# Kernel optimization log

Measured on AMD Instinct MI355X. Metric: run time of the kernel, lower is better.

## Reference

```python
import jax, jax.numpy as jnp
import numpy as np

N, NA, LAYERS = 8, 4, 4
NTOT = N + NA
DIM = 2 ** NTOT
B = 1024

# Diagonal of the fixed CZ brick layer (CZ is diagonal, so one elementwise pass per layer).
# Qubit 0 is the most-significant bit of the state index (tensorcircuit convention).
def _cz_diag():
    idx = np.arange(DIM)
    bits = (idx[None, :] >> (NTOT - 1 - np.arange(NTOT)[:, None])) & 1  # [NTOT, DIM]
    par = np.zeros(DIM, dtype=np.int64)
    for i in range(NTOT // 2):
        par += bits[2 * i] * bits[2 * i + 1]
    for i in range((NTOT - 1) // 2):
        par += bits[2 * i + 1] * bits[2 * i + 2]
    return jnp.asarray(1.0 - 2.0 * (par % 2), dtype=jnp.complex64)

CZ_DIAG = _cz_diag()

def _apply_1q(state, U, q):
    # state: [B, DIM]; apply 2x2 unitary U on qubit q (batched over samples)
    l, r = 2 ** q, 2 ** (NTOT - q - 1)
    s = state.reshape(-1, l, 2, r)
    return jnp.einsum('ij,bljr->blir', U, s).reshape(-1, DIM)

def _back_circuit(state, params):
    # hardware-efficient ansatz: per layer RX,RY on every qubit, then CZ bricks
    for lay in range(LAYERS):
        off = 2 * NTOT * lay
        for q in range(NTOT):
            th = params[off + q] * 0.5
            c = jnp.cos(th).astype(jnp.complex64)
            ms = (-1j) * jnp.sin(th).astype(jnp.complex64)
            Rx = jnp.stack([jnp.stack([c, ms]), jnp.stack([ms, c])])
            state = _apply_1q(state, Rx, q)
            th = params[off + NTOT + q] * 0.5
            c, s = jnp.cos(th), jnp.sin(th)
            Ry = jnp.stack([jnp.stack([c, -s]), jnp.stack([s, c])]).astype(jnp.complex64)
            state = _apply_1q(state, Ry, q)
        state = state * CZ_DIAG
    return state

def setup_inputs() -> dict:
    key = jax.random.key(0)
    k1, k2, k3, k4 = jax.random.split(key, 4)
    return {
        'inputs_re': jax.random.normal(k1, (B, DIM), jnp.float32),
        'inputs_im': jax.random.normal(k2, (B, DIM), jnp.float32),
        'params': jax.random.normal(k3, (2 * NTOT * LAYERS,), jnp.float32),
        'u': jax.random.uniform(k4, (B,), jnp.float32),
    }

def reference(inputs_re, inputs_im, params, u):
    state = (inputs_re + 1j * inputs_im).astype(jnp.complex64)
    full = _back_circuit(state, params)                      # [B, 2^n_tot]
    s3 = full.reshape(B, 2 ** NA, 2 ** N)                    # [B, 2^na, 2^n]
    probs = jnp.sum(s3.real ** 2 + s3.imag ** 2, axis=2)     # ancilla outcome probs
    cdf = jnp.cumsum(probs, axis=1)
    thresh = u * cdf[:, -1]                                  # inverse-CDF multinomial
    m = jnp.argmax(cdf >= thresh[:, None], axis=1)           # [B] sampled outcome
    post = s3[jnp.arange(B), m]                              # [B, 2^n] collapsed state
    norm = jnp.sqrt(jnp.sum(post.real ** 2 + post.imag ** 2, axis=1, keepdims=True))
    post = post / norm
    return jnp.stack([post.real, post.imag], axis=-1)        # [B, 2^n, 2]
```

## Files before the change

### kernel.cpp

```cpp
#include <hip/hip_runtime.h>
#include <math.h>

#define NTOT   12
#define DIM    4096
#define LAYERS 4
#define NB     1024
#define SPAD   4160

typedef float v2f __attribute__((ext_vector_type(2)));

template<int G>
__device__ __forceinline__ void gate_pk64(v2f (&x)[64], v2f P1, v2f P2) {
#pragma unroll
    for (int p = 0; p < 32; ++p) {
        const int j0 = ((p >> G) << (G + 1)) | (p & ((1 << G) - 1));
        const int j1 = j0 | (1 << G);
        const v2f x0 = x[j0], x1 = x[j1];
        v2f t, u;
        asm("v_pk_mul_f32 %0, %1, %2 op_sel:[1,1] op_sel_hi:[1,0] neg_hi:[1,0]"
            : "=v"(t) : "v"(P2), "v"(x1));
        asm("v_pk_fma_f32 %0, %1, %2, %0 op_sel:[1,0,0] op_sel_hi:[1,1,1] neg_lo:[1,0,0] neg_hi:[1,0,0]"
            : "+v"(t) : "v"(P1), "v"(x1));
        asm("v_pk_fma_f32 %0, %1, %2, %0 op_sel:[0,1,0] op_sel_hi:[0,0,1] neg_lo:[1,0,0]"
            : "+v"(t) : "v"(P2), "v"(x0));
        asm("v_pk_fma_f32 %0, %1, %2, %0 op_sel:[0,0,0] op_sel_hi:[0,1,1]"
            : "+v"(t) : "v"(P1), "v"(x0));
        asm("v_pk_mul_f32 %0, %1, %2 op_sel:[0,1] op_sel_hi:[0,0] neg_hi:[1,0]"
            : "=v"(u) : "v"(P2), "v"(x1));
        asm("v_pk_fma_f32 %0, %1, %2, %0 op_sel:[0,0,0] op_sel_hi:[0,1,1]"
            : "+v"(u) : "v"(P1), "v"(x1));
        asm("v_pk_fma_f32 %0, %1, %2, %0 op_sel:[1,1,0] op_sel_hi:[1,0,1] neg_hi:[1,0,0]"
            : "+v"(u) : "v"(P2), "v"(x0));
        asm("v_pk_fma_f32 %0, %1, %2, %0 op_sel:[1,0,0] op_sel_hi:[1,1,1]"
            : "+v"(u) : "v"(P1), "v"(x0));
        x[j0] = t; x[j1] = u;
    }
}

__device__ __forceinline__ void apply6(v2f (&x)[64], const float4* gco, int top) {
    float4 c;
    c = gco[top - 0]; gate_pk64<0>(x, (v2f){c.x, c.y}, (v2f){c.z, c.w});
    c = gco[top - 1]; gate_pk64<1>(x, (v2f){c.x, c.y}, (v2f){c.z, c.w});
    c = gco[top - 2]; gate_pk64<2>(x, (v2f){c.x, c.y}, (v2f){c.z, c.w});
    c = gco[top - 3]; gate_pk64<3>(x, (v2f){c.x, c.y}, (v2f){c.z, c.w});
    c = gco[top - 4]; gate_pk64<4>(x, (v2f){c.x, c.y}, (v2f){c.z, c.w});
    c = gco[top - 5]; gate_pk64<5>(x, (v2f){c.x, c.y}, (v2f){c.z, c.w});
}

__device__ __forceinline__ void applyCZ64(v2f (&x)[64], unsigned long long mask) {
#pragma unroll
    for (int j = 0; j < 64; ++j) {
        const unsigned int w = (j < 32) ? (unsigned int)mask : (unsigned int)(mask >> 32);
        const unsigned int sw = (w << (31 - (j & 31))) & 0x80000000u;
        x[j].x = __uint_as_float(__float_as_uint(x[j].x) ^ sw);
        x[j].y = __uint_as_float(__float_as_uint(x[j].y) ^ sw);
    }
}

#define KPAR 0xB8B7B8484748B848ULL

__global__ __launch_bounds__(64, 1) void qddpm_kernel(
    const float* __restrict__ in_re,
    const float* __restrict__ in_im,
    const float* __restrict__ params,
    const float* __restrict__ uu,
    float* __restrict__ out)
{
    __shared__ v2f    S[SPAD];
    __shared__ float4 gco[48];
    __shared__ float  sprob[16];

    const int b = blockIdx.x;
    const int l = threadIdx.x;
    const float uval = uu[b];

    if (l < 48) {
        const int lay = l / 12, q = l - lay * 12;
        float c1, s1, c2, s2;
        sincosf(params[lay * 24 + q] * 0.5f, &s1, &c1);
        sincosf(params[lay * 24 + 12 + q] * 0.5f, &s2, &c2);
        gco[l] = make_float4(c1 * c2, c1 * s2, s1 * s2, s1 * c2);
    }

    const unsigned long long parl = ((KPAR >> l) & 1ULL) ? ~0ULL : 0ULL;
    const unsigned long long maskQ =
        KPAR ^ parl ^ ((l & 1)  ? 0xFFFFFFFF00000000ULL : 0ULL);
    const unsigned long long maskP =
        KPAR ^ parl ^ ((l & 32) ? 0xAAAAAAAAAAAAAAAAULL : 0ULL);

    v2f x[64];
    v2f acc2 = (v2f){0.0f, 0.0f};

#pragma unroll 1
    for (int lay = 0; lay < LAYERS; ++lay) {
        if (lay == 0) {
            const float* re = in_re + (size_t)b * DIM + l;
            const float* im = in_im + (size_t)b * DIM + l;
#pragma unroll
            for (int j = 0; j < 64; ++j)
                x[j] = (v2f){re[64 * j], im[64 * j]};
        } else {
#pragma unroll
            for (int j = 0; j < 64; ++j) x[j] = S[65 * j + l];
        }
        apply6(x, gco, lay * 12 + 5);
#pragma unroll
        for (int j = 0; j < 64; ++j) S[65 * j + l] = x[j];

#pragma unroll
        for (int j = 0; j < 64; ++j) x[j] = S[65 * l + j];
        apply6(x, gco, lay * 12 + 11);
        applyCZ64(x, maskQ);
        if (lay == LAYERS - 1) {
#pragma unroll
            for (int j = 0; j < 64; ++j) acc2 += x[j] * x[j];
        }
#pragma unroll
        for (int j = 0; j < 64; ++j) S[65 * l + j] = x[j];
    }
    (void)maskP;

    {
        float partial = acc2.x + acc2.y;
        partial += __shfl_down(partial, 2, 4);
        partial += __shfl_down(partial, 1, 4);
        if ((l & 3) == 0) sprob[l >> 2] = partial;
    }

    {
        float cdf[16];
        float a = 0.0f;
#pragma unroll
        for (int i = 0; i < 16; ++i) { a += sprob[i]; cdf[i] = a; }
        const float thresh = uval * a;
        int m = 0;
#pragma unroll
        for (int i = 15; i >= 0; --i) { if (cdf[i] >= thresh) m = i; }
        const float rn = 1.0f / sqrtf(sprob[m]);

        float2* o2 = (float2*)out + (size_t)b * 256;
#pragma unroll
        for (int c = 0; c < 4; ++c) {
            const v2f amp = S[260 * m + 65 * c + l];
            o2[c * 64 + l] = make_float2(amp.x * rn, amp.y * rn);
        }
    }
}

extern "C" void kernel_launch(void* const* d_in, const int* in_sizes, int n_in,
                              void* d_out, int out_size, void* d_ws, size_t ws_size,
                              hipStream_t stream) {
    const float* in_re  = (const float*)d_in[0];
    const float* in_im  = (const float*)d_in[1];
    const float* params = (const float*)d_in[2];
    const float* u      = (const float*)d_in[3];
    float* out = (float*)d_out;
    qddpm_kernel<<<NB, 64, 0, stream>>>(in_re, in_im, params, u, out);
}
```

Measured before the change: 116.9 us.

## Alternate state layout between half-layers to halve LDS transposes

The state is now loaded contiguously per thread with float4 global loads, so each thread starts holding a row instead of a strided column. The layer loop is split into eight half-layer steps that alternate between the two layouts. It transposes through shared memory only once per layer, and the CZ sign mask is picked to match the current layout (maskQ or maskP). This cuts LDS write/read round trips and strided global loads, at the cost of a slightly more complex control flow with runtime layout selection.

```diff
diff --git a/kernel.cpp b/kernel.cpp
--- a/kernel.cpp
+++ b/kernel.cpp
@@ -1,13 +1,12 @@
 #include <hip/hip_runtime.h>
 #include <math.h>
 
-#define NTOT   12
 #define DIM    4096
-#define LAYERS 4
 #define NB     1024
 #define SPAD   4160
 
 typedef float v2f __attribute__((ext_vector_type(2)));
+typedef unsigned long long ull;
 
 template<int G>
 __device__ __forceinline__ void gate_pk64(v2f (&x)[64], v2f P1, v2f P2) {
@@ -37,21 +36,11 @@
     }
 }
 
-__device__ __forceinline__ void apply6(v2f (&x)[64], const float4* gco, int top) {
-    float4 c;
-    c = gco[top - 0]; gate_pk64<0>(x, (v2f){c.x, c.y}, (v2f){c.z, c.w});
-    c = gco[top - 1]; gate_pk64<1>(x, (v2f){c.x, c.y}, (v2f){c.z, c.w});
-    c = gco[top - 2]; gate_pk64<2>(x, (v2f){c.x, c.y}, (v2f){c.z, c.w});
-    c = gco[top - 3]; gate_pk64<3>(x, (v2f){c.x, c.y}, (v2f){c.z, c.w});
-    c = gco[top - 4]; gate_pk64<4>(x, (v2f){c.x, c.y}, (v2f){c.z, c.w});
-    c = gco[top - 5]; gate_pk64<5>(x, (v2f){c.x, c.y}, (v2f){c.z, c.w});
-}
-
-__device__ __forceinline__ void applyCZ64(v2f (&x)[64], unsigned long long mask) {
+__device__ __forceinline__ void applyCZ64(v2f (&x)[64], ull mask) {
 #pragma unroll
     for (int j = 0; j < 64; ++j) {
-        const unsigned int w = (j < 32) ? (unsigned int)mask : (unsigned int)(mask >> 32);
-        const unsigned int sw = (w << (31 - (j & 31))) & 0x80000000u;
+        const unsigned w = (j < 32) ? (unsigned)mask : (unsigned)(mask >> 32);
+        const unsigned sw = (w << (31 - (j & 31))) & 0x80000000u;
         x[j].x = __uint_as_float(__float_as_uint(x[j].x) ^ sw);
         x[j].y = __uint_as_float(__float_as_uint(x[j].y) ^ sw);
     }
@@ -74,6 +63,20 @@
     const int l = threadIdx.x;
     const float uval = uu[b];
 
+    v2f x[64];
+    {
+        const float4* re4 = (const float4*)(in_re + (size_t)b * DIM + l * 64);
+        const float4* im4 = (const float4*)(in_im + (size_t)b * DIM + l * 64);
+#pragma unroll
+        for (int q = 0; q < 16; ++q) {
+            const float4 vr = re4[q];
+            const float4 vi = im4[q];
+            x[4 * q + 0] = (v2f){vr.x, vi.x};
+            x[4 * q + 1] = (v2f){vr.y, vi.y};
+            x[4 * q + 2] = (v2f){vr.z, vi.z};
+            x[4 * q + 3] = (v2f){vr.w, vi.w};
+        }
+    }
     if (l < 48) {
         const int lay = l / 12, q = l - lay * 12;
         float c1, s1, c2, s2;
@@ -81,52 +84,49 @@
         sincosf(params[lay * 24 + 12 + q] * 0.5f, &s2, &c2);
         gco[l] = make_float4(c1 * c2, c1 * s2, s1 * s2, s1 * c2);
     }
-
-    const unsigned long long parl = ((KPAR >> l) & 1ULL) ? ~0ULL : 0ULL;
-    const unsigned long long maskQ =
-        KPAR ^ parl ^ ((l & 1)  ? 0xFFFFFFFF00000000ULL : 0ULL);
-    const unsigned long long maskP =
-        KPAR ^ parl ^ ((l & 32) ? 0xAAAAAAAAAAAAAAAAULL : 0ULL);
-
-    v2f x[64];
-    v2f acc2 = (v2f){0.0f, 0.0f};
+    const ull parl  = ((KPAR >> l) & 1ULL) ? ~0ULL : 0ULL;
+    const ull maskQ = KPAR ^ parl ^ ((l & 1)  ? 0xFFFFFFFF00000000ULL : 0ULL);
+    const ull maskP = KPAR ^ parl ^ ((l & 32) ? 0xAAAAAAAAAAAAAAAAULL : 0ULL);
 
 #pragma unroll 1
-    for (int lay = 0; lay < LAYERS; ++lay) {
-        if (lay == 0) {
-            const float* re = in_re + (size_t)b * DIM + l;
-            const float* im = in_im + (size_t)b * DIM + l;
+    for (int k = 0; k < 8; ++k) {
+        const int isQ = (~(k ^ (k >> 1))) & 1;
+        if (k & 1) {
+            if (!isQ) {
 #pragma unroll
-            for (int j = 0; j < 64; ++j)
-                x[j] = (v2f){re[64 * j], im[64 * j]};
-        } else {
+                for (int j = 0; j < 64; ++j) S[65 * l + j] = x[j];
 #pragma unroll
-            for (int j = 0; j < 64; ++j) x[j] = S[65 * j + l];
+                for (int j = 0; j < 64; ++j) x[j] = S[65 * j + l];
+            } else {
+#pragma unroll
+                for (int j = 0; j < 64; ++j) S[65 * j + l] = x[j];
+#pragma unroll
+                for (int j = 0; j < 64; ++j) x[j] = S[65 * l + j];
+            }
         }
-        apply6(x, gco, lay * 12 + 5);
-#pragma unroll
-        for (int j = 0; j < 64; ++j) S[65 * j + l] = x[j];
+        const int top = 12 * (k >> 1) + (isQ ? 11 : 5);
+        { float4 c;
+          c = gco[top - 0]; gate_pk64<0>(x, (v2f){c.x, c.y}, (v2f){c.z, c.w});
+          c = gco[top - 1]; gate_pk64<1>(x, (v2f){c.x, c.y}, (v2f){c.z, c.w});
+          c = gco[top - 2]; gate_pk64<2>(x, (v2f){c.x, c.y}, (v2f){c.z, c.w});
+          c = gco[top - 3]; gate_pk64<3>(x, (v2f){c.x, c.y}, (v2f){c.z, c.w});
+          c = gco[top - 4]; gate_pk64<4>(x, (v2f){c.x, c.y}, (v2f){c.z, c.w});
+          c = gco[top - 5]; gate_pk64<5>(x, (v2f){c.x, c.y}, (v2f){c.z, c.w}); }
+        if (k & 1)
+            applyCZ64(x, isQ ? maskQ : maskP);
+    }
 
 #pragma unroll
-        for (int j = 0; j < 64; ++j) x[j] = S[65 * l + j];
-        apply6(x, gco, lay * 12 + 11);
-        applyCZ64(x, maskQ);
-        if (lay == LAYERS - 1) {
+    for (int j = 0; j < 64; ++j) S[65 * l + j] = x[j];
+    {
+        v2f a2 = (v2f){0.0f, 0.0f};
 #pragma unroll
-            for (int j = 0; j < 64; ++j) acc2 += x[j] * x[j];
-        }
-#pragma unroll
-        for (int j = 0; j < 64; ++j) S[65 * l + j] = x[j];
+        for (int j = 0; j < 64; ++j) a2 += x[j] * x[j];
+        float p = a2.x + a2.y;
+        p += __shfl_down(p, 2, 4);
+        p += __shfl_down(p, 1, 4);
+        if ((l & 3) == 0) sprob[l >> 2] = p;
     }
-    (void)maskP;
-
-    {
-        float partial = acc2.x + acc2.y;
-        partial += __shfl_down(partial, 2, 4);
-        partial += __shfl_down(partial, 1, 4);
-        if ((l & 3) == 0) sprob[l >> 2] = partial;
-    }
-
     {
         float cdf[16];
         float a = 0.0f;
@@ -137,12 +137,11 @@
 #pragma unroll
         for (int i = 15; i >= 0; --i) { if (cdf[i] >= thresh) m = i; }
         const float rn = 1.0f / sqrtf(sprob[m]);
-
         float2* o2 = (float2*)out + (size_t)b * 256;
 #pragma unroll
-        for (int c = 0; c < 4; ++c) {
-            const v2f amp = S[260 * m + 65 * c + l];
-            o2[c * 64 + l] = make_float2(amp.x * rn, amp.y * rn);
+        for (int q = 0; q < 4; ++q) {
+            const v2f amp = S[260 * m + 65 * q + l];
+            o2[q * 64 + l] = make_float2(amp.x * rn, amp.y * rn);
         }
     }
 }
```

New measurement: 116.3 us. Within noise of the previous version (-0.5%).
